# Optimization experiments

Measured on AMD Instinct MI355X. Metric: run time of the kernel, lower is better.

Reference implementation:

```python
import jax, jax.numpy as jnp
import numpy as np

L = 2          # num_layers
D = 2048       # embed_dim
HQ = 16        # num_q_heads
HK = 4         # num_kv_heads
HD = D // HQ   # head_size = 128
G = HQ // HK   # q_to_kv_ratio = 4
P = 8192       # embed_dim_proj
V = 32000      # vocab_size
B = 1
S = 2048
EPS = 1e-5
THETA = 500000.0
NEG = -1e30


def setup_inputs() -> dict:
    key = jax.random.key(0)
    ks = jax.random.split(key, 8)
    s = 0.02
    return {
        "tokens": jax.random.randint(ks[0], (B, S), 0, V, dtype=jnp.int32),
        "embed": jax.random.normal(ks[1], (V, D), jnp.float32) * s,
        "attn_norm_w": jnp.ones((L, D), jnp.float32),
        "qkv_w": jax.random.normal(ks[2], (L, D, D + 2 * HK * HD), jnp.float32) * s,
        "attn_out_w": jax.random.normal(ks[3], (L, D, D), jnp.float32) * s,
        "mlp_norm_w": jnp.ones((L, D), jnp.float32),
        "mlp_in_w": jax.random.normal(ks[4], (L, D, 2 * P), jnp.float32) * s,
        "mlp_out_w": jax.random.normal(ks[5], (L, P, D), jnp.float32) * s,
        "final_norm_w": jnp.ones((D,), jnp.float32),
        "lm_head_w": jax.random.normal(ks[6], (D, V), jnp.float32) * s,
    }


def _rms(x, w):
    return w * (x * jax.lax.rsqrt(jnp.mean(x * x, axis=-1, keepdims=True) + EPS))


def _rope_cos_sin():
    inv = 1.0 / (THETA ** (jnp.arange(0, HD, 2, dtype=jnp.float32) / HD))  # [HD/2]
    ang = jnp.arange(S, dtype=jnp.float32)[:, None] * inv[None, :]         # [S, HD/2]
    return jnp.cos(ang), jnp.sin(ang)


def _rope(t, cos, sin):
    # t: [B,S,H,HD]; interleaved complex rotation on (even, odd) pairs
    x = t.reshape(t.shape[:-1] + (HD // 2, 2))
    x0, x1 = x[..., 0], x[..., 1]
    c = cos[None, :, None, :]
    sn = sin[None, :, None, :]
    out = jnp.stack([x0 * c - x1 * sn, x0 * sn + x1 * c], axis=-1)
    return out.reshape(t.shape)


def _layer(x, nw1, wqkv, wo, nw2, wi, wmo, cos, sin, mask):
    # attention block (pre-norm, residual)
    h = _rms(x, nw1)
    qkv = h @ wqkv
    q = qkv[..., :D].reshape(B, S, HQ, HD)
    k = qkv[..., D:D + HK * HD].reshape(B, S, HK, HD)
    v = qkv[..., D + HK * HD:].reshape(B, S, HK, HD)
    q = _rope(q, cos, sin)
    k = _rope(k, cos, sin)
    # GQA: repeat_interleave along head dim
    k = jnp.repeat(k, G, axis=2)
    v = jnp.repeat(v, G, axis=2)
    scores = jnp.einsum('bqhd,bkhd->bhqk', q, k) / np.float32(np.sqrt(HD))
    scores = jnp.where(mask, scores, NEG)
    attn = jax.nn.softmax(scores, axis=-1)
    o = jnp.einsum('bhqk,bkhd->bqhd', attn, v).reshape(B, S, D)
    x = x + o @ wo
    # SwiGLU block (pre-norm, residual)
    h = _rms(x, nw2)
    gu = h @ wi
    gate, up = gu[..., :P], gu[..., P:]
    x = x + (jax.nn.silu(gate) * up) @ wmo
    return x


def reference(tokens, embed, attn_norm_w, qkv_w, attn_out_w, mlp_norm_w,
              mlp_in_w, mlp_out_w, final_norm_w, lm_head_w):
    cos, sin = _rope_cos_sin()
    mask = jnp.tril(jnp.ones((S, S), dtype=bool))  # offset=0 prefill -> causal
    x = embed[tokens]  # [B,S,D]
    for i in range(L):
        x = _layer(x, attn_norm_w[i], qkv_w[i], attn_out_w[i],
                   mlp_norm_w[i], mlp_in_w[i], mlp_out_w[i], cos, sin, mask)
    return _rms(x, final_norm_w) @ lm_head_w  # [B,S,V]
```

## Files before the change

### kernel.cpp

```cpp
#include <hip/hip_runtime.h>
#include <math.h>

#define S_LEN 2048
#define DMODEL 2048
#define NHQ 16
#define NHK 4
#define HDIM 128
#define PDIM 8192
#define VOCAB 32000
#define NQKV 3072
#define EPSI 1e-5f

typedef unsigned short u16;
typedef unsigned int u32;
typedef __bf16 bf16x8 __attribute__((ext_vector_type(8)));
typedef float f32x4 __attribute__((ext_vector_type(4)));

__device__ __forceinline__ u16 f2bf(float f){
  u32 u = __builtin_bit_cast(u32, f);
  u += 0x7fffu + ((u >> 16) & 1u);
  return (u16)(u >> 16);
}
__device__ __forceinline__ float bf2f(u16 h){
  u32 u = ((u32)h) << 16;
  return __builtin_bit_cast(float, u);
}
__device__ __forceinline__ bf16x8 ld8(const u16* p){
  return __builtin_bit_cast(bf16x8, *(const uint4*)p);
}
__device__ __forceinline__ f32x4 mfma16(bf16x8 a, bf16x8 b, f32x4 c){
  return __builtin_amdgcn_mfma_f32_16x16x32_bf16(a, b, c, 0, 0, 0);
}

#define GLOAD_LDS16(gp, lp) __builtin_amdgcn_global_load_lds( \
    (__attribute__((address_space(1))) void*)(gp), \
    (__attribute__((address_space(3))) void*)(lp), 16, 0, 0)

__device__ __forceinline__ bf16x8 lds_frag(const u16* Lb, int R, int g){
  const int Rp = R >> 1;
  const int s8 = (((R & 1) << 2) | g) ^ (Rp & 7);
  return ld8(Lb + Rp * 64 + s8 * 8);
}
__device__ __forceinline__ void stage_sw(const u16* base, long row0, int kstride, int kt,
                                         int q, u16* Ldst_waveuniform){
  const int Rp = q >> 3;
  const int u = (q & 7) ^ (Rp & 7);
  const int R = (Rp << 1) | (u >> 2);
  const u16* gp = base + (row0 + R) * (long)kstride + kt + ((u & 3) << 3);
  GLOAD_LDS16(gp, Ldst_waveuniform);
}

__device__ __forceinline__ void map_bmn(int id0, int nwg, int nbn, int G,
                                        int& bm, int& bn){
  const int cpx = nwg >> 3;
  const int id = (id0 & 7) * cpx + (id0 >> 3);
  const int bmi = id % G;
  const int r2 = id / G;
  bn = r2 % nbn;
  bm = (r2 / nbn) * G + bmi;
}

__global__ void k_embed(const int* __restrict__ tok, const float* __restrict__ emb,
                        float* __restrict__ x){
  const int s = blockIdx.x, t = threadIdx.x;
  const long r = tok[s];
  const float4* src = (const float4*)(emb + r * DMODEL);
  float4* dst = (float4*)(x + (long)s * DMODEL);
  dst[t] = src[t];
  dst[t + 256] = src[t + 256];
}

__global__ void k_rmsnorm(const float* __restrict__ x, const float* __restrict__ w,
                          u16* __restrict__ out){
  const int s = blockIdx.x, t = threadIdx.x;
  const float4* xr = (const float4*)(x + (long)s * DMODEL);
  const float4 a = xr[t], b = xr[t + 256];
  float ss = a.x*a.x + a.y*a.y + a.z*a.z + a.w*a.w
           + b.x*b.x + b.y*b.y + b.z*b.z + b.w*b.w;
  #pragma unroll
  for (int off = 32; off > 0; off >>= 1) ss += __shfl_down(ss, off, 64);
  __shared__ float part[4];
  if ((t & 63) == 0) part[t >> 6] = ss;
  __syncthreads();
  const float r = rsqrtf((part[0] + part[1] + part[2] + part[3]) * (1.f / 2048.f) + EPSI);
  const float4* wr = (const float4*)w;
  const float4 wa = wr[t], wb = wr[t + 256];
  uint2 ua, ub;
  ua.x = (u32)f2bf(a.x*r*wa.x) | ((u32)f2bf(a.y*r*wa.y) << 16);
  ua.y = (u32)f2bf(a.z*r*wa.z) | ((u32)f2bf(a.w*r*wa.w) << 16);
  ub.x = (u32)f2bf(b.x*r*wb.x) | ((u32)f2bf(b.y*r*wb.y) << 16);
  ub.y = (u32)f2bf(b.z*r*wb.z) | ((u32)f2bf(b.w*r*wb.w) << 16);
  *(uint2*)(out + (long)s * DMODEL + 4 * t) = ua;
  *(uint2*)(out + (long)s * DMODEL + 1024 + 4 * t) = ub;
}

__global__ void k_red2rms(float* __restrict__ x, const float* __restrict__ p0,
                          const float* __restrict__ p1, const float* __restrict__ w,
                          u16* __restrict__ out){
  const int s = blockIdx.x, t = threadIdx.x;
  const long base = (long)s * DMODEL;
  float4 a = ((const float4*)(x + base))[t];
  float4 b = ((const float4*)(x + base))[t + 256];
  const float4 a0 = ((const float4*)(p0 + base))[t];
  const float4 b0 = ((const float4*)(p0 + base))[t + 256];
  const float4 a1 = ((const float4*)(p1 + base))[t];
  const float4 b1 = ((const float4*)(p1 + base))[t + 256];
  a.x += a0.x + a1.x; a.y += a0.y + a1.y; a.z += a0.z + a1.z; a.w += a0.w + a1.w;
  b.x += b0.x + b1.x; b.y += b0.y + b1.y; b.z += b0.z + b1.z; b.w += b0.w + b1.w;
  ((float4*)(x + base))[t] = a;
  ((float4*)(x + base))[t + 256] = b;
  float ss = a.x*a.x + a.y*a.y + a.z*a.z + a.w*a.w
           + b.x*b.x + b.y*b.y + b.z*b.z + b.w*b.w;
  #pragma unroll
  for (int off = 32; off > 0; off >>= 1) ss += __shfl_down(ss, off, 64);
  __shared__ float part[4];
  if ((t & 63) == 0) part[t >> 6] = ss;
  __syncthreads();
  const float r = rsqrtf((part[0] + part[1] + part[2] + part[3]) * (1.f / 2048.f) + EPSI);
  const float4* wr = (const float4*)w;
  const float4 wa = wr[t], wb = wr[t + 256];
  uint2 ua, ub;
  ua.x = (u32)f2bf(a.x*r*wa.x) | ((u32)f2bf(a.y*r*wa.y) << 16);
  ua.y = (u32)f2bf(a.z*r*wa.z) | ((u32)f2bf(a.w*r*wa.w) << 16);
  ub.x = (u32)f2bf(b.x*r*wb.x) | ((u32)f2bf(b.y*r*wb.y) << 16);
  ub.y = (u32)f2bf(b.z*r*wb.z) | ((u32)f2bf(b.w*r*wb.w) << 16);
  *(uint2*)(out + base + 4 * t) = ua;
  *(uint2*)(out + base + 1024 + 4 * t) = ub;
}

__global__ __launch_bounds__(256) void k_convT(const float* __restrict__ W,
                                               u16* __restrict__ Wt, int N, int K){
  const int n0 = blockIdx.x * 64, k0 = blockIdx.y * 64;
  const int t = threadIdx.x;
  __shared__ u16 T[64][72];
  const int r = t >> 4, c = (t & 15) << 2;
  #pragma unroll
  for (int p = 0; p < 4; ++p){
    const int k = p * 16 + r;
    const float4 v = *(const float4*)(W + (long)(k0 + k) * N + n0 + c);
    T[c + 0][k] = f2bf(v.x);
    T[c + 1][k] = f2bf(v.y);
    T[c + 2][k] = f2bf(v.z);
    T[c + 3][k] = f2bf(v.w);
  }
  __syncthreads();
  const int nr = t >> 3, kc = (t & 7) << 3;
  #pragma unroll
  for (int p = 0; p < 2; ++p){
    const int n = p * 32 + nr;
    *(uint4*)(Wt + (long)(n0 + n) * K + k0 + kc) = *(const uint4*)(&T[n][kc]);
  }
}

__global__ __launch_bounds__(256) void k_convTmi(const float* __restrict__ W,
                                                 u16* __restrict__ Wt, int N, int K){
  const int n0 = blockIdx.x * 64, k0 = blockIdx.y * 64;
  const int t = threadIdx.x;
  __shared__ u16 T[64][72];
  const int r = t >> 4, c = (t & 15) << 2;
  #pragma unroll
  for (int p = 0; p < 4; ++p){
    const int k = p * 16 + r;
    const float4 v = *(const float4*)(W + (long)(k0 + k) * N + n0 + c);
    T[c + 0][k] = f2bf(v.x);
    T[c + 1][k] = f2bf(v.y);
    T[c + 2][k] = f2bf(v.z);
    T[c + 3][k] = f2bf(v.w);
  }
  __syncthreads();
  int drow0;
  if (n0 < PDIM) drow0 = (n0 >> 7) * 256 + (n0 & 127);
  else { const int m0 = n0 - PDIM; drow0 = (m0 >> 7) * 256 + 128 + (m0 & 127); }
  const int nr = t >> 3, kc = (t & 7) << 3;
  #pragma unroll
  for (int p = 0; p < 2; ++p){
    const int n = p * 32 + nr;
    *(uint4*)(Wt + (long)(drow0 + n) * K + k0 + kc) = *(const uint4*)(&T[n][kc]);
  }
}

__global__ __launch_bounds__(256) void k_transV(const u16* __restrict__ qkv,
                                                u16* __restrict__ vT){
  const int s0 = blockIdx.x * 64, d0 = blockIdx.y * 64, kh = blockIdx.z;
  const int t = threadIdx.x;
  __shared__ u16 T[64][72];
  #pragma unroll
  for (int p = 0; p < 4; ++p){
    const int s = p * 16 + (t >> 4);
    const int c = (t & 15) * 4;
    const uint2 v = *(const uint2*)(qkv + (long)(s0 + s) * NQKV + DMODEL + 512 + kh * HDIM + d0 + c);
    T[c + 0][s] = (u16)(v.x);
    T[c + 1][s] = (u16)(v.x >> 16);
    T[c + 2][s] = (u16)(v.y);
    T[c + 3][s] = (u16)(v.y >> 16);
  }
  __syncthreads();
  #pragma unroll
  for (int p = 0; p < 2; ++p){
    const int d = p * 32 + (t >> 3);
    *(uint4*)(vT + ((long)kh * HDIM + d0 + d) * S_LEN + s0 + (t & 7) * 8) =
        *(const uint4*)(&T[d][(t & 7) * 8]);
  }
}

template<int OUT_BF16, int RES>
__global__ __launch_bounds__(256) void k_gemm(const u16* __restrict__ A, const u16* __restrict__ Bt,
                                              void* C, const float* Rs,
                                              int M, int N, int K, int nbn, int G){
  int bm, bn;
  map_bmn(blockIdx.x, gridDim.x, nbn, G, bm, bn);
  const int t = threadIdx.x;
  const int w = t >> 6, lane = t & 63, l15 = lane & 15, g = lane >> 4;
  const int wr = w >> 1, wc = w & 1;
  __shared__ u16 As[4096];
  __shared__ u16 Bs[4096];
  f32x4 acc[4][4] = {};
  const long arow = (long)bm * 128;
  const long brow = (long)bn * 128;
  for (int kt = 0; kt < K; kt += 32){
    __syncthreads();
    #pragma unroll
    for (int c = 0; c < 2; ++c){
      const int q0 = ((w << 1) | c) << 6;
      const int q  = q0 | lane;
      stage_sw(A,  arow, K, kt, q, As + q0 * 8);
      stage_sw(Bt, brow, K, kt, q, Bs + q0 * 8);
    }
    __syncthreads();
    bf16x8 af[4], bfr[4];
    #pragma unroll
    for (int i = 0; i < 4; ++i)
      af[i] = lds_frag(As, wr * 64 + i * 16 + l15, g);
    #pragma unroll
    for (int i = 0; i < 4; ++i)
      bfr[i] = lds_frag(Bs, wc * 64 + i * 16 + l15, g);
    #pragma unroll
    for (int mi = 0; mi < 4; ++mi)
      #pragma unroll
      for (int ni = 0; ni < 4; ++ni)
        acc[mi][ni] = mfma16(af[mi], bfr[ni], acc[mi][ni]);
  }
  const int row0 = bm * 128 + wr * 64, col0 = bn * 128 + wc * 64;
  #pragma unroll
  for (int mi = 0; mi < 4; ++mi){
    #pragma unroll
    for (int ni = 0; ni < 4; ++ni){
      #pragma unroll
      for (int r = 0; r < 4; ++r){
        const long ri = row0 + mi * 16 + g * 4 + r;
        const long ci = col0 + ni * 16 + l15;
        float v = acc[mi][ni][r];
        if (RES) v += Rs[ri * N + ci];
        if (OUT_BF16) ((u16*)C)[ri * N + ci] = f2bf(v);
        else          ((float*)C)[ri * N + ci] = v;
      }
    }
  }
}

__global__ __launch_bounds__(256) void k_gemmsk(const u16* __restrict__ A,
                                                const u16* __restrict__ Bt,
                                                float* __restrict__ P,
                                                int M, int N, int K, int nbn, int G){
  const int ks = blockIdx.y;
  const int KH = K >> 1;
  A  += (long)ks * KH;
  Bt += (long)ks * KH;
  P  += (long)ks * M * N;
  int bm, bn;
  map_bmn(blockIdx.x, gridDim.x, nbn, G, bm, bn);
  const int t = threadIdx.x;
  const int w = t >> 6, lane = t & 63, l15 = lane & 15, g = lane >> 4;
  const int wr = w >> 1, wc = w & 1;
  __shared__ u16 As[4096];
  __shared__ u16 Bs[4096];
  f32x4 acc[4][4] = {};
  const long arow = (long)bm * 128;
  const long brow = (long)bn * 128;
  for (int kt = 0; kt < KH; kt += 32){
    __syncthreads();
    #pragma unroll
    for (int c = 0; c < 2; ++c){
      const int q0 = ((w << 1) | c) << 6;
      const int q  = q0 | lane;
      stage_sw(A,  arow, K, kt, q, As + q0 * 8);
      stage_sw(Bt, brow, K, kt, q, Bs + q0 * 8);
    }
    __syncthreads();
    bf16x8 af[4], bfr[4];
    #pragma unroll
    for (int i = 0; i < 4; ++i)
      af[i] = lds_frag(As, wr * 64 + i * 16 + l15, g);
    #pragma unroll
    for (int i = 0; i < 4; ++i)
      bfr[i] = lds_frag(Bs, wc * 64 + i * 16 + l15, g);
    #pragma unroll
    for (int mi = 0; mi < 4; ++mi)
      #pragma unroll
      for (int ni = 0; ni < 4; ++ni)
        acc[mi][ni] = mfma16(af[mi], bfr[ni], acc[mi][ni]);
  }
  const int row0 = bm * 128 + wr * 64, col0 = bn * 128 + wc * 64;
  #pragma unroll
  for (int mi = 0; mi < 4; ++mi){
    #pragma unroll
    for (int ni = 0; ni < 4; ++ni){
      #pragma unroll
      for (int r = 0; r < 4; ++r){
        const long ri = row0 + mi * 16 + g * 4 + r;
        const long ci = col0 + ni * 16 + l15;
        P[ri * N + ci] = acc[mi][ni][r];
      }
    }
  }
}

template<int OUT_BF16>
__global__ __launch_bounds__(1024, 4) void k_gemmX(const u16* __restrict__ A,
                                                   const u16* __restrict__ Bt,
                                                   void* C, int M, int N, int K){
  __shared__ u16 L[65536];
  const int t = threadIdx.x;
  const int w = t >> 6, lane = t & 63, l15 = lane & 15, g = lane >> 4;
  const int wr = w >> 2, wc = w & 3;
  const int nbm = M >> 8;
  int id = blockIdx.x;
  {
    const int cpx = gridDim.x >> 3;
    id = (id & 7) * cpx + (id >> 3);
  }
  const int bm = id % nbm, bn = id / nbm;
  const int NT = K >> 5;

  const int Rp0 = t >> 3;
  const int u0  = (t & 7) ^ (Rp0 & 7);
  const int R0  = (Rp0 << 1) | (u0 >> 2);
  const int kc0 = (u0 & 3) << 3;
  const u16* pA = A  + ((long)bm * 256 + R0) * (long)K + kc0;
  const u16* pB = Bt + ((long)bn * 256 + R0) * (long)K + kc0;
  const int w0 = (t & ~63) * 8;

  auto stage = [&](int s){
    u16* d = L + s * 16384;
    GLOAD_LDS16(pA, d + w0);
    GLOAD_LDS16(pB, d + 8192 + w0);
    pA += 32; pB += 32;
  };

  stage(0); stage(1); stage(2);
  asm volatile("s_waitcnt vmcnt(4)" ::: "memory");
  __builtin_amdgcn_s_barrier();

  f32x4 acc[4][4] = {};
  for (int tt = 0; tt < NT; ++tt){
    const int slot = tt & 3;
    const u16* sA = L + slot * 16384;
    const u16* sB = sA + 8192;
    bf16x8 af[4], bfr[4];
    #pragma unroll
    for (int mi = 0; mi < 4; ++mi)
      af[mi] = lds_frag(sA, wr * 64 + mi * 16 + l15, g);
    #pragma unroll
    for (int ni = 0; ni < 4; ++ni)
      bfr[ni] = lds_frag(sB, wc * 64 + ni * 16 + l15, g);
    if (tt + 3 < NT) stage((tt + 3) & 3);
    asm volatile("s_waitcnt lgkmcnt(0)" ::: "memory");
    if (tt + 3 < NT)      asm volatile("s_waitcnt vmcnt(4)" ::: "memory");
    else if (tt + 2 < NT) asm volatile("s_waitcnt vmcnt(2)" ::: "memory");
    else if (tt + 1 < NT) asm volatile("s_waitcnt vmcnt(0)" ::: "memory");
    __builtin_amdgcn_s_barrier();
    __builtin_amdgcn_s_setprio(1);
    #pragma unroll
    for (int mi = 0; mi < 4; ++mi)
      #pragma unroll
      for (int ni = 0; ni < 4; ++ni)
        acc[mi][ni] = mfma16(af[mi], bfr[ni], acc[mi][ni]);
    __builtin_amdgcn_s_setprio(0);
  }
  const int row0 = bm * 256 + wr * 64, col0 = bn * 256 + wc * 64;
  #pragma unroll
  for (int mi = 0; mi < 4; ++mi){
    #pragma unroll
    for (int ni = 0; ni < 4; ++ni){
      #pragma unroll
      for (int r = 0; r < 4; ++r){
        const long ri = row0 + mi * 16 + g * 4 + r;
        const long ci = col0 + ni * 16 + l15;
        const float v = acc[mi][ni][r];
        if (OUT_BF16) ((u16*)C)[ri * N + ci] = f2bf(v);
        else          ((float*)C)[ri * N + ci] = v;
      }
    }
  }
}

__global__ __launch_bounds__(1024, 4) void k_gemmXswi(const u16* __restrict__ A,
                                                      const u16* __restrict__ Bt,
                                                      u16* __restrict__ O,
                                                      int M, int K){
  __shared__ u16 L[65536];
  const int t = threadIdx.x;
  const int w = t >> 6, lane = t & 63, l15 = lane & 15, g = lane >> 4;
  const int wr = w >> 2, wc = w & 3;
  const int nbm = M >> 8;
  int id = blockIdx.x;
  {
    const int cpx = gridDim.x >> 3;
    id = (id & 7) * cpx + (id >> 3);
  }
  const int bm = id % nbm, bn = id / nbm;
  const int NT = K >> 5;

  const int Rp0 = t >> 3;
  const int u0  = (t & 7) ^ (Rp0 & 7);
  const int R0  = (Rp0 << 1) | (u0 >> 2);
  const int kc0 = (u0 & 3) << 3;
  const u16* pA = A  + ((long)bm * 256 + R0) * (long)K + kc0;
  const u16* pB = Bt + ((long)bn * 256 + R0) * (long)K + kc0;
  const int w0 = (t & ~63) * 8;

  auto stage = [&](int s){
    u16* d = L + s * 16384;
    GLOAD_LDS16(pA, d + w0);
    GLOAD_LDS16(pB, d + 8192 + w0);
    pA += 32; pB += 32;
  };

  stage(0); stage(1); stage(2);
  asm volatile("s_waitcnt vmcnt(4)" ::: "memory");
  __builtin_amdgcn_s_barrier();

  f32x4 acc[4][4] = {};
  for (int tt = 0; tt < NT; ++tt){
    const int slot = tt & 3;
    const u16* sA = L + slot * 16384;
    const u16* sB = sA + 8192;
    bf16x8 af[4], bfr[4];
    #pragma unroll
    for (int mi = 0; mi < 4; ++mi)
      af[mi] = lds_frag(sA, wr * 64 + mi * 16 + l15, g);
    #pragma unroll
    for (int ni = 0; ni < 4; ++ni)
      bfr[ni] = lds_frag(sB, wc * 64 + ni * 16 + l15, g);
    if (tt + 3 < NT) stage((tt + 3) & 3);
    asm volatile("s_waitcnt lgkmcnt(0)" ::: "memory");
    if (tt + 3 < NT)      asm volatile("s_waitcnt vmcnt(4)" ::: "memory");
    else if (tt + 2 < NT) asm volatile("s_waitcnt vmcnt(2)" ::: "memory");
    else if (tt + 1 < NT) asm volatile("s_waitcnt vmcnt(0)" ::: "memory");
    __builtin_amdgcn_s_barrier();
    __builtin_amdgcn_s_setprio(1);
    #pragma unroll
    for (int mi = 0; mi < 4; ++mi)
      #pragma unroll
      for (int ni = 0; ni < 4; ++ni)
        acc[mi][ni] = mfma16(af[mi], bfr[ni], acc[mi][ni]);
    __builtin_amdgcn_s_setprio(0);
  }
  __syncthreads();
  float* U = (float*)L;
  if (wc >= 2){
    const int base = ((wr << 1) | (wc - 2)) * 4096;
    #pragma unroll
    for (int mi = 0; mi < 4; ++mi)
      #pragma unroll
      for (int ni = 0; ni < 4; ++ni)
        #pragma unroll
        for (int r = 0; r < 4; ++r)
          U[base + (mi * 16 + g * 4 + r) * 64 + ni * 16 + l15] = acc[mi][ni][r];
  }
  __syncthreads();
  if (wc < 2){
    const int base = ((wr << 1) | wc) * 4096;
    #pragma unroll
    for (int mi = 0; mi < 4; ++mi){
      #pragma unroll
      for (int ni = 0; ni < 4; ++ni){
        #pragma unroll
        for (int r = 0; r < 4; ++r){
          const float gv = acc[mi][ni][r];
          const float uv = U[base + (mi * 16 + g * 4 + r) * 64 + ni * 16 + l15];
          const float ov = gv / (1.f + __expf(-gv)) * uv;
          const long ri = bm * 256 + wr * 64 + mi * 16 + g * 4 + r;
          const int ci = bn * 128 + wc * 64 + ni * 16 + l15;
          O[ri * PDIM + ci] = f2bf(ov);
        }
      }
    }
  }
}

__global__ void k_rope(u16* __restrict__ qkv){
  const int idx = blockIdx.x * 256 + threadIdx.x;
  const int i = idx & 63;
  const int head = (idx >> 6) % 20;
  const int s = idx / (64 * 20);
  const long base = (long)s * NQKV + (head < NHQ ? head * HDIM : DMODEL + (head - NHQ) * HDIM);
  u32* p = (u32*)(qkv + base + 2 * i);
  const u32 v = *p;
  const float x0 = bf2f((u16)(v & 0xffffu)), x1 = bf2f((u16)(v >> 16));
  const float ang = (float)s * exp2f(-0.29580575889569023f * (float)i);
  float sn, cs;
  sincosf(ang, &sn, &cs);
  const float y0 = x0 * cs - x1 * sn;
  const float y1 = x0 * sn + x1 * cs;
  *p = (u32)f2bf(y0) | ((u32)f2bf(y1) << 16);
}

__global__ __launch_bounds__(256) void k_attn(const u16* __restrict__ qkv,
                                              const u16* __restrict__ vT,
                                              u16* __restrict__ o){
  const int id = blockIdx.x;
  const int xcd = id & 7, j = id >> 3;
  const int kh = xcd >> 1;
  const int h  = (kh << 2) + ((xcd & 1) << 1) + (j & 1);
  const int qb = 31 - (j >> 1);
  const int t = threadIdx.x, w = t >> 6, lane = t & 63, l15 = lane & 15, g = lane >> 4;
  __shared__ u16 Ks[2][8192];
  __shared__ u16 Vs[2][8192];
  __shared__ u16 Ps[4][16 * 72];
  const int q0 = qb * 64 + w * 16;
  bf16x8 aq[4];
  #pragma unroll
  for (int d0 = 0; d0 < 4; ++d0)
    aq[d0] = ld8(qkv + (long)(q0 + l15) * NQKV + h * HDIM + d0 * 32 + g * 8);
  f32x4 acc_o[8] = {};
  float mst[4], lst[4];
  #pragma unroll
  for (int r = 0; r < 4; ++r){ mst[r] = -1e30f; lst[r] = 0.f; }
  const float scale = 0.08838834764831843f;

  auto stageK = [&](int kt, int b){
    #pragma unroll
    for (int p = 0; p < 4; ++p){
      const int q = p * 256 + t;
      const int r = q >> 4, u = q & 15;
      const u16* gp = qkv + (long)(kt * 64 + r) * NQKV + DMODEL + kh * HDIM + ((u ^ (r & 15)) << 3);
      GLOAD_LDS16(gp, Ks[b] + (p * 256 + (t & ~63)) * 8);
    }
  };
  auto stageV = [&](int kt, int b){
    #pragma unroll
    for (int p = 0; p < 4; ++p){
      const int q = p * 256 + t;
      const int r = q >> 3, u = q & 7;
      const u16* gp = vT + ((long)kh * HDIM + r) * S_LEN + kt * 64 + ((u ^ (r & 7)) << 3);
      GLOAD_LDS16(gp, Vs[b] + (p * 256 + (t & ~63)) * 8);
    }
  };

  const int nkt = qb + 1;
  stageK(0, 0); stageV(0, 0);
  for (int kt = 0; kt < nkt; ++kt){
    const int kv0 = kt << 6;
    __builtin_amdgcn_s_barrier();
    if (kt + 1 < nkt){
      stageK(kt + 1, (kt + 1) & 1);
      stageV(kt + 1, (kt + 1) & 1);
      asm volatile("s_waitcnt vmcnt(8)" ::: "memory");
    } else {
      asm volatile("s_waitcnt vmcnt(0)" ::: "memory");
    }
    __builtin_amdgcn_s_barrier();
    const u16* K_ = Ks[kt & 1];
    const u16* V_ = Vs[kt & 1];
    f32x4 sacc[4] = {};
    #pragma unroll
    for (int d0 = 0; d0 < 4; ++d0){
      #pragma unroll
      for (int j2 = 0; j2 < 4; ++j2){
        const bf16x8 bk = ld8(K_ + (j2 * 16 + l15) * 128 + ((((d0 << 2) | g) ^ l15) << 3));
        sacc[j2] = mfma16(aq[d0], bk, sacc[j2]);
      }
    }
    float p[4][4], scl[4];
    #pragma unroll
    for (int r = 0; r < 4; ++r){
      const int qrow = q0 + g * 4 + r;
      float mx = -1e30f;
      #pragma unroll
      for (int j2 = 0; j2 < 4; ++j2){
        float sv = sacc[j2][r] * scale;
        sv = (kv0 + j2 * 16 + l15 <= qrow) ? sv : -1e30f;
        p[j2][r] = sv;
        mx = fmaxf(mx, sv);
      }
      #pragma unroll
      for (int off = 1; off < 16; off <<= 1) mx = fmaxf(mx, __shfl_xor(mx, off, 64));
      const float mnew = fmaxf(mst[r], mx);
      scl[r] = __expf(mst[r] - mnew);
      float rs = 0.f;
      #pragma unroll
      for (int j2 = 0; j2 < 4; ++j2){ p[j2][r] = __expf(p[j2][r] - mnew); rs += p[j2][r]; }
      #pragma unroll
      for (int off = 1; off < 16; off <<= 1) rs += __shfl_xor(rs, off, 64);
      lst[r] = lst[r] * scl[r] + rs;
      mst[r] = mnew;
    }
    #pragma unroll
    for (int n = 0; n < 8; ++n)
      #pragma unroll
      for (int r = 0; r < 4; ++r)
        acc_o[n][r] *= scl[r];
    #pragma unroll
    for (int j2 = 0; j2 < 4; ++j2)
      #pragma unroll
      for (int r = 0; r < 4; ++r)
        Ps[w][(g * 4 + r) * 72 + j2 * 16 + l15] = f2bf(p[j2][r]);
    #pragma unroll
    for (int kk = 0; kk < 2; ++kk){
      const bf16x8 pa = ld8(Ps[w] + l15 * 72 + kk * 32 + g * 8);
      #pragma unroll
      for (int n = 0; n < 8; ++n){
        const int row = n * 16 + l15;
        const bf16x8 bv = ld8(V_ + row * 64 + ((((kk << 2) | g) ^ (l15 & 7)) << 3));
        acc_o[n] = mfma16(pa, bv, acc_o[n]);
      }
    }
    asm volatile("s_waitcnt lgkmcnt(0)" ::: "memory");
  }
  #pragma unroll
  for (int n = 0; n < 8; ++n){
    #pragma unroll
    for (int r = 0; r < 4; ++r){
      const float ov = acc_o[n][r] / lst[r];
      o[(long)(q0 + g * 4 + r) * DMODEL + h * HDIM + n * 16 + l15] = f2bf(ov);
    }
  }
}

extern "C" void kernel_launch(void* const* d_in, const int* in_sizes, int n_in,
                              void* d_out, int out_size, void* d_ws, size_t ws_size,
                              hipStream_t stream){
  const int*   tokens       = (const int*)d_in[0];
  const float* embed        = (const float*)d_in[1];
  const float* attn_norm_w  = (const float*)d_in[2];
  const float* qkv_w        = (const float*)d_in[3];
  const float* attn_out_w   = (const float*)d_in[4];
  const float* mlp_norm_w   = (const float*)d_in[5];
  const float* mlp_in_w     = (const float*)d_in[6];
  const float* mlp_out_w    = (const float*)d_in[7];
  const float* final_norm_w = (const float*)d_in[8];
  const float* lm_head_w    = (const float*)d_in[9];

  char* ws = (char*)d_ws;
  float* xf  = (float*)(ws);
  u16* hbf   = (u16*)(ws + 16777216);
  u16* qkvb  = (u16*)(ws + 25165824);
  u16* obf   = (u16*)(ws + 37748736);
  u16* gub   = (u16*)(ws + 46137344);
  u16* hb2   = (u16*)(ws + 113246208);
  u16* wbuf  = (u16*)(ws + 146800640);
  u16* vTb   = (u16*)(ws + 277872640);
  float* pp  = (float*)gub;

  k_embed<<<S_LEN, 256, 0, stream>>>(tokens, embed, xf);
  k_rmsnorm<<<S_LEN, 256, 0, stream>>>(xf, attn_norm_w, hbf);
  for (int l = 0; l < 2; ++l){
    k_convT<<<dim3(NQKV/64, DMODEL/64), 256, 0, stream>>>(
        qkv_w + (long)l * DMODEL * NQKV, wbuf, NQKV, DMODEL);
    k_gemm<1,0><<<(S_LEN/128) * (NQKV/128), 256, 0, stream>>>(
        hbf, wbuf, qkvb, nullptr, S_LEN, NQKV, DMODEL, NQKV/128, 4);
    k_rope<<<(S_LEN * 20 * 64) / 256, 256, 0, stream>>>(qkvb);
    k_transV<<<dim3(S_LEN/64, 2, 4), 256, 0, stream>>>(qkvb, vTb);
    k_attn<<<512, 256, 0, stream>>>(qkvb, vTb, obf);
    k_convT<<<dim3(DMODEL/64, DMODEL/64), 256, 0, stream>>>(
        attn_out_w + (long)l * DMODEL * DMODEL, wbuf, DMODEL, DMODEL);
    k_gemm<0,1><<<(S_LEN/128) * (DMODEL/128), 256, 0, stream>>>(
        obf, wbuf, xf, xf, S_LEN, DMODEL, DMODEL, DMODEL/128, 4);
    k_rmsnorm<<<S_LEN, 256, 0, stream>>>(xf, mlp_norm_w + (long)l * DMODEL, hbf);
    k_convTmi<<<dim3((2*PDIM)/64, DMODEL/64), 256, 0, stream>>>(
        mlp_in_w + (long)l * DMODEL * 2 * PDIM, wbuf, 2*PDIM, DMODEL);
    k_gemmXswi<<<(S_LEN/256) * ((2*PDIM)/256), 1024, 0, stream>>>(
        hbf, wbuf, hb2, S_LEN, DMODEL);
    k_convT<<<dim3(DMODEL/64, PDIM/64), 256, 0, stream>>>(
        mlp_out_w + (long)l * PDIM * DMODEL, wbuf, DMODEL, PDIM);
    k_gemmsk<<<dim3((S_LEN/128) * (DMODEL/128), 2), 256, 0, stream>>>(
        hb2, wbuf, pp, S_LEN, DMODEL, PDIM, DMODEL/128, 2);
    k_red2rms<<<S_LEN, 256, 0, stream>>>(
        xf, pp, pp + (long)S_LEN * DMODEL,
        (l == 0) ? (attn_norm_w + DMODEL) : final_norm_w, hbf);
  }
  k_convT<<<dim3(VOCAB/64, DMODEL/64), 256, 0, stream>>>(lm_head_w, wbuf, VOCAB, DMODEL);
  k_gemmX<0><<<(S_LEN/256) * (VOCAB/256), 1024, 0, stream>>>(
      hbf, wbuf, (float*)d_out, S_LEN, VOCAB, DMODEL);
}
```

Measured before the change: 1.374 ms.

## Replace 1024-thread 256x256 GEMMs with 256-thread 128x256 tiles for MLP-in and LM head

The large MLP-in (SwiGLU) and LM-head GEMMs move from 16-wave 256x256 tiles with 4-stage LDS buffering to 4-wave 128x256 tiles with 3-stage buffering. Each wave now computes a 128x64 output with 32 accumulators, and blocks are ordered through a grouped bm/bn mapping. The intent is better per-wave MFMA reuse of A fragments, lower LDS footprint and better L2 locality. In exchange it raises register pressure, shortens the prefetch depth and reduces occupancy flexibility.

```diff
diff --git a/kernel.cpp b/kernel.cpp
--- a/kernel.cpp
+++ b/kernel.cpp
@@ -316,70 +316,73 @@
 }
 
 template<int OUT_BF16>
-__global__ __launch_bounds__(1024, 4) void k_gemmX(const u16* __restrict__ A,
-                                                   const u16* __restrict__ Bt,
-                                                   void* C, int M, int N, int K){
-  __shared__ u16 L[65536];
+__global__ __launch_bounds__(256, 2) void k_gemmY(const u16* __restrict__ A,
+                                                  const u16* __restrict__ Bt,
+                                                  void* C, int M, int N, int K,
+                                                  int nbn, int G){
+  __shared__ u16 L[36864];
   const int t = threadIdx.x;
   const int w = t >> 6, lane = t & 63, l15 = lane & 15, g = lane >> 4;
-  const int wr = w >> 2, wc = w & 3;
-  const int nbm = M >> 8;
-  int id = blockIdx.x;
-  {
-    const int cpx = gridDim.x >> 3;
-    id = (id & 7) * cpx + (id >> 3);
-  }
-  const int bm = id % nbm, bn = id / nbm;
+  int bm, bn;
+  map_bmn(blockIdx.x, gridDim.x, nbn, G, bm, bn);
   const int NT = K >> 5;
 
   const int Rp0 = t >> 3;
   const int u0  = (t & 7) ^ (Rp0 & 7);
   const int R0  = (Rp0 << 1) | (u0 >> 2);
   const int kc0 = (u0 & 3) << 3;
-  const u16* pA = A  + ((long)bm * 256 + R0) * (long)K + kc0;
+  const u16* pA = A  + ((long)bm * 128 + R0) * (long)K + kc0;
   const u16* pB = Bt + ((long)bn * 256 + R0) * (long)K + kc0;
   const int w0 = (t & ~63) * 8;
 
   auto stage = [&](int s){
-    u16* d = L + s * 16384;
-    GLOAD_LDS16(pA, d + w0);
-    GLOAD_LDS16(pB, d + 8192 + w0);
+    u16* dA = L + s * 12288;
+    u16* dB = dA + 4096;
+    GLOAD_LDS16(pA,                dA + w0);
+    GLOAD_LDS16(pA + (long)64 * K, dA + 2048 + w0);
+    GLOAD_LDS16(pB,                 dB + w0);
+    GLOAD_LDS16(pB + (long)64 * K,  dB + 2048 + w0);
+    GLOAD_LDS16(pB + (long)128 * K, dB + 4096 + w0);
+    GLOAD_LDS16(pB + (long)192 * K, dB + 6144 + w0);
     pA += 32; pB += 32;
   };
 
-  stage(0); stage(1); stage(2);
-  asm volatile("s_waitcnt vmcnt(4)" ::: "memory");
+  stage(0); stage(1);
+  asm volatile("s_waitcnt vmcnt(6)" ::: "memory");
   __builtin_amdgcn_s_barrier();
 
-  f32x4 acc[4][4] = {};
+  f32x4 acc[8][4] = {};
+  int slot = 0;
   for (int tt = 0; tt < NT; ++tt){
-    const int slot = tt & 3;
-    const u16* sA = L + slot * 16384;
-    const u16* sB = sA + 8192;
-    bf16x8 af[4], bfr[4];
-    #pragma unroll
-    for (int mi = 0; mi < 4; ++mi)
-      af[mi] = lds_frag(sA, wr * 64 + mi * 16 + l15, g);
+    const u16* sA = L + slot * 12288;
+    const u16* sB = sA + 4096;
+    bf16x8 af[8], bfr[4];
+    #pragma unroll
+    for (int mi = 0; mi < 8; ++mi)
+      af[mi] = lds_frag(sA, mi * 16 + l15, g);
     #pragma unroll
     for (int ni = 0; ni < 4; ++ni)
-      bfr[ni] = lds_frag(sB, wc * 64 + ni * 16 + l15, g);
-    if (tt + 3 < NT) stage((tt + 3) & 3);
+      bfr[ni] = lds_frag(sB, w * 64 + ni * 16 + l15, g);
+    if (tt + 2 < NT){
+      int s2 = slot + 2; if (s2 >= 3) s2 -= 3;
+      stage(s2);
+    }
     asm volatile("s_waitcnt lgkmcnt(0)" ::: "memory");
-    if (tt + 3 < NT)      asm volatile("s_waitcnt vmcnt(4)" ::: "memory");
-    else if (tt + 2 < NT) asm volatile("s_waitcnt vmcnt(2)" ::: "memory");
+    if (tt + 2 < NT)      asm volatile("s_waitcnt vmcnt(6)" ::: "memory");
     else if (tt + 1 < NT) asm volatile("s_waitcnt vmcnt(0)" ::: "memory");
     __builtin_amdgcn_s_barrier();
     __builtin_amdgcn_s_setprio(1);
     #pragma unroll
-    for (int mi = 0; mi < 4; ++mi)
+    for (int mi = 0; mi < 8; ++mi)
       #pragma unroll
       for (int ni = 0; ni < 4; ++ni)
         acc[mi][ni] = mfma16(af[mi], bfr[ni], acc[mi][ni]);
     __builtin_amdgcn_s_setprio(0);
-  }
-  const int row0 = bm * 256 + wr * 64, col0 = bn * 256 + wc * 64;
-  #pragma unroll
-  for (int mi = 0; mi < 4; ++mi){
+    ++slot; if (slot == 3) slot = 0;
+  }
+  const int row0 = bm * 128, col0 = bn * 256 + w * 64;
+  #pragma unroll
+  for (int mi = 0; mi < 8; ++mi){
     #pragma unroll
     for (int ni = 0; ni < 4; ++ni){
       #pragma unroll
@@ -394,74 +397,76 @@
   }
 }
 
-__global__ __launch_bounds__(1024, 4) void k_gemmXswi(const u16* __restrict__ A,
-                                                      const u16* __restrict__ Bt,
-                                                      u16* __restrict__ O,
-                                                      int M, int K){
-  __shared__ u16 L[65536];
+__global__ __launch_bounds__(256, 2) void k_gemmYswi(const u16* __restrict__ A,
+                                                     const u16* __restrict__ Bt,
+                                                     u16* __restrict__ O,
+                                                     int M, int K, int nbn, int G){
+  __shared__ u16 L[36864];
   const int t = threadIdx.x;
   const int w = t >> 6, lane = t & 63, l15 = lane & 15, g = lane >> 4;
-  const int wr = w >> 2, wc = w & 3;
-  const int nbm = M >> 8;
-  int id = blockIdx.x;
-  {
-    const int cpx = gridDim.x >> 3;
-    id = (id & 7) * cpx + (id >> 3);
-  }
-  const int bm = id % nbm, bn = id / nbm;
+  int bm, bn;
+  map_bmn(blockIdx.x, gridDim.x, nbn, G, bm, bn);
   const int NT = K >> 5;
 
   const int Rp0 = t >> 3;
   const int u0  = (t & 7) ^ (Rp0 & 7);
   const int R0  = (Rp0 << 1) | (u0 >> 2);
   const int kc0 = (u0 & 3) << 3;
-  const u16* pA = A  + ((long)bm * 256 + R0) * (long)K + kc0;
+  const u16* pA = A  + ((long)bm * 128 + R0) * (long)K + kc0;
   const u16* pB = Bt + ((long)bn * 256 + R0) * (long)K + kc0;
   const int w0 = (t & ~63) * 8;
 
   auto stage = [&](int s){
-    u16* d = L + s * 16384;
-    GLOAD_LDS16(pA, d + w0);
-    GLOAD_LDS16(pB, d + 8192 + w0);
+    u16* dA = L + s * 12288;
+    u16* dB = dA + 4096;
+    GLOAD_LDS16(pA,                dA + w0);
+    GLOAD_LDS16(pA + (long)64 * K, dA + 2048 + w0);
+    GLOAD_LDS16(pB,                 dB + w0);
+    GLOAD_LDS16(pB + (long)64 * K,  dB + 2048 + w0);
+    GLOAD_LDS16(pB + (long)128 * K, dB + 4096 + w0);
+    GLOAD_LDS16(pB + (long)192 * K, dB + 6144 + w0);
     pA += 32; pB += 32;
   };
 
-  stage(0); stage(1); stage(2);
-  asm volatile("s_waitcnt vmcnt(4)" ::: "memory");
+  stage(0); stage(1);
+  asm volatile("s_waitcnt vmcnt(6)" ::: "memory");
   __builtin_amdgcn_s_barrier();
 
-  f32x4 acc[4][4] = {};
+  f32x4 acc[8][4] = {};
+  int slot = 0;
   for (int tt = 0; tt < NT; ++tt){
-    const int slot = tt & 3;
-    const u16* sA = L + slot * 16384;
-    const u16* sB = sA + 8192;
-    bf16x8 af[4], bfr[4];
-    #pragma unroll
-    for (int mi = 0; mi < 4; ++mi)
-      af[mi] = lds_frag(sA, wr * 64 + mi * 16 + l15, g);
+    const u16* sA = L + slot * 12288;
+    const u16* sB = sA + 4096;
+    bf16x8 af[8], bfr[4];
+    #pragma unroll
+    for (int mi = 0; mi < 8; ++mi)
+      af[mi] = lds_frag(sA, mi * 16 + l15, g);
     #pragma unroll
     for (int ni = 0; ni < 4; ++ni)
-      bfr[ni] = lds_frag(sB, wc * 64 + ni * 16 + l15, g);
-    if (tt + 3 < NT) stage((tt + 3) & 3);
+      bfr[ni] = lds_frag(sB, w * 64 + ni * 16 + l15, g);
+    if (tt + 2 < NT){
+      int s2 = slot + 2; if (s2 >= 3) s2 -= 3;
+      stage(s2);
+    }
     asm volatile("s_waitcnt lgkmcnt(0)" ::: "memory");
-    if (tt + 3 < NT)      asm volatile("s_waitcnt vmcnt(4)" ::: "memory");
-    else if (tt + 2 < NT) asm volatile("s_waitcnt vmcnt(2)" ::: "memory");
+    if (tt + 2 < NT)      asm volatile("s_waitcnt vmcnt(6)" ::: "memory");
     else if (tt + 1 < NT) asm volatile("s_waitcnt vmcnt(0)" ::: "memory");
     __builtin_amdgcn_s_barrier();
     __builtin_amdgcn_s_setprio(1);
     #pragma unroll
-    for (int mi = 0; mi < 4; ++mi)
+    for (int mi = 0; mi < 8; ++mi)
       #pragma unroll
       for (int ni = 0; ni < 4; ++ni)
         acc[mi][ni] = mfma16(af[mi], bfr[ni], acc[mi][ni]);
     __builtin_amdgcn_s_setprio(0);
+    ++slot; if (slot == 3) slot = 0;
   }
   __syncthreads();
   float* U = (float*)L;
-  if (wc >= 2){
-    const int base = ((wr << 1) | (wc - 2)) * 4096;
-    #pragma unroll
-    for (int mi = 0; mi < 4; ++mi)
+  if (w >= 2){
+    const int base = (w - 2) * 8192;
+    #pragma unroll
+    for (int mi = 0; mi < 8; ++mi)
       #pragma unroll
       for (int ni = 0; ni < 4; ++ni)
         #pragma unroll
@@ -469,10 +474,10 @@
           U[base + (mi * 16 + g * 4 + r) * 64 + ni * 16 + l15] = acc[mi][ni][r];
   }
   __syncthreads();
-  if (wc < 2){
-    const int base = ((wr << 1) | wc) * 4096;
-    #pragma unroll
-    for (int mi = 0; mi < 4; ++mi){
+  if (w < 2){
+    const int base = w * 8192;
+    #pragma unroll
+    for (int mi = 0; mi < 8; ++mi){
       #pragma unroll
       for (int ni = 0; ni < 4; ++ni){
         #pragma unroll
@@ -480,8 +485,8 @@
           const float gv = acc[mi][ni][r];
           const float uv = U[base + (mi * 16 + g * 4 + r) * 64 + ni * 16 + l15];
           const float ov = gv / (1.f + __expf(-gv)) * uv;
-          const long ri = bm * 256 + wr * 64 + mi * 16 + g * 4 + r;
-          const int ci = bn * 128 + wc * 64 + ni * 16 + l15;
+          const long ri = bm * 128 + mi * 16 + g * 4 + r;
+          const int ci = bn * 128 + w * 64 + ni * 16 + l15;
           O[ri * PDIM + ci] = f2bf(ov);
         }
       }
@@ -670,8 +675,8 @@
     k_rmsnorm<<<S_LEN, 256, 0, stream>>>(xf, mlp_norm_w + (long)l * DMODEL, hbf);
     k_convTmi<<<dim3((2*PDIM)/64, DMODEL/64), 256, 0, stream>>>(
         mlp_in_w + (long)l * DMODEL * 2 * PDIM, wbuf, 2*PDIM, DMODEL);
-    k_gemmXswi<<<(S_LEN/256) * ((2*PDIM)/256), 1024, 0, stream>>>(
-        hbf, wbuf, hb2, S_LEN, DMODEL);
+    k_gemmYswi<<<(S_LEN/128) * ((2*PDIM)/256), 256, 0, stream>>>(
+        hbf, wbuf, hb2, S_LEN, DMODEL, (2*PDIM)/256, 4);
     k_convT<<<dim3(DMODEL/64, PDIM/64), 256, 0, stream>>>(
         mlp_out_w + (long)l * PDIM * DMODEL, wbuf, DMODEL, PDIM);
     k_gemmsk<<<dim3((S_LEN/128) * (DMODEL/128), 2), 256, 0, stream>>>(
@@ -681,6 +686,6 @@
         (l == 0) ? (attn_norm_w + DMODEL) : final_norm_w, hbf);
   }
   k_convT<<<dim3(VOCAB/64, DMODEL/64), 256, 0, stream>>>(lm_head_w, wbuf, VOCAB, DMODEL);
-  k_gemmX<0><<<(S_LEN/256) * (VOCAB/256), 1024, 0, stream>>>(
-      hbf, wbuf, (float*)d_out, S_LEN, VOCAB, DMODEL);
-}
+  k_gemmY<0><<<(S_LEN/128) * (VOCAB/256), 256, 0, stream>>>(
+      hbf, wbuf, (float*)d_out, S_LEN, VOCAB, DMODEL, VOCAB/256, 4);
+}
```

Result: slower. 1.402 ms (+2.0%).
